# Kernel tuning notes

Measured on AMD Instinct MI355X. Metric: run time of the kernel, lower is better.

Reference implementation:

```python
import jax, jax.numpy as jnp
import numpy as np

N_NODES = 100000
N_EDGES = 400000
F_IN = 128
HEADS = 4
C1 = 64   # conv1 out per head
C2 = 128  # conv2 out per head
G = 2048  # num graphs
FP = 2048
HID = 64
NEG_SLOPE = 0.2


def _gat_conv(x, edge_index, W, a_src, a_dst, b, heads, ch):
    """PyG-style GATConv with self-loops, concat=True."""
    n = x.shape[0]
    loops = jnp.arange(n, dtype=edge_index.dtype)
    src = jnp.concatenate([edge_index[0], loops])
    dst = jnp.concatenate([edge_index[1], loops])
    h = (x @ W).reshape(n, heads, ch)                      # [N,H,C]
    e_src = jnp.sum(h * a_src, axis=-1)                    # [N,H]
    e_dst = jnp.sum(h * a_dst, axis=-1)                    # [N,H]
    logits = jax.nn.leaky_relu(e_src[src] + e_dst[dst], NEG_SLOPE)  # [E,H]
    m = jax.ops.segment_max(logits, dst, num_segments=n)   # per-dst max
    p = jnp.exp(logits - m[dst])
    denom = jax.ops.segment_sum(p, dst, num_segments=n)
    alpha = p / denom[dst]                                 # [E,H]
    out = jax.ops.segment_sum(h[src] * alpha[:, :, None], dst, num_segments=n)
    return out.reshape(n, heads * ch) + b


def setup_inputs() -> dict:
    key = jax.random.key(0)
    ks = jax.random.split(key, 16)
    s = 0.05
    inp = {
        "x": jax.random.normal(ks[0], (N_NODES, F_IN), jnp.float32),
        "edge_index": jax.random.randint(ks[1], (2, N_EDGES), 0, N_NODES, jnp.int32),
        "batch": jnp.sort(jax.random.randint(ks[2], (N_NODES,), 0, G, jnp.int32)),
        "fp": jax.random.normal(ks[3], (G, FP), jnp.float32),
        "W1": jax.random.normal(ks[4], (F_IN, HEADS * C1), jnp.float32) * s,
        "a_src1": jax.random.normal(ks[5], (HEADS, C1), jnp.float32) * s,
        "a_dst1": jax.random.normal(ks[6], (HEADS, C1), jnp.float32) * s,
        "b1": jnp.zeros((HEADS * C1,), jnp.float32),
        "W2": jax.random.normal(ks[7], (HEADS * C1, HEADS * C2), jnp.float32) * s,
        "a_src2": jax.random.normal(ks[8], (HEADS, C2), jnp.float32) * s,
        "a_dst2": jax.random.normal(ks[9], (HEADS, C2), jnp.float32) * s,
        "b2": jnp.zeros((HEADS * C2,), jnp.float32),
        "Wfp": jax.random.normal(ks[10], (FP, HID), jnp.float32) * s,
        "bfp": jnp.zeros((HID,), jnp.float32),
        "Wfc1": jax.random.normal(ks[11], (HEADS * C2 + HID, HID), jnp.float32) * s,
        "bfc1": jnp.zeros((HID,), jnp.float32),
        "Wfc2": jax.random.normal(ks[12], (HID, 1), jnp.float32) * s,
        "bfc2": jnp.zeros((1,), jnp.float32),
    }
    return inp


def reference(x, edge_index, batch, fp, W1, a_src1, a_dst1, b1, W2, a_src2, a_dst2, b2,
              Wfp, bfp, Wfc1, bfc1, Wfc2, bfc2):
    h = _gat_conv(x, edge_index, W1, a_src1, a_dst1, b1, HEADS, C1)
    h = jax.nn.elu(h)
    h = _gat_conv(h, edge_index, W2, a_src2, a_dst2, b2, HEADS, C2)
    h = jax.nn.elu(h)
    # global mean pool over graphs
    sums = jax.ops.segment_sum(h, batch, num_segments=G)
    counts = jax.ops.segment_sum(jnp.ones((h.shape[0], 1), h.dtype), batch, num_segments=G)
    pooled = sums / jnp.maximum(counts, 1.0)               # [G, 512]
    fph = fp @ Wfp + bfp                                   # [G, 64]
    z = jnp.concatenate([pooled, fph], axis=1)             # [G, 576]
    z = jax.nn.relu(z @ Wfc1 + bfc1)
    # dropout is identity in eval mode
    return z @ Wfc2 + bfc2                                 # [G, 1]
```

## Files before the change

### kernel.cpp

```cpp
#include <hip/hip_runtime.h>
#include <math.h>

#define NEG_SLOPE 0.2f

typedef __attribute__((ext_vector_type(8))) short bf16x8;
typedef __attribute__((ext_vector_type(4))) float f32x4;
typedef __attribute__((ext_vector_type(2))) float f32x2;

__device__ __forceinline__ float b2f(short s) {
  return __uint_as_float(((unsigned int)(unsigned short)s) << 16);
}
__device__ __forceinline__ unsigned short f2b_rne(float f) {
  unsigned int u = __float_as_uint(f);
  u = (u + 0x7FFF + ((u >> 16) & 1)) >> 16;
  return (unsigned short)u;
}

__device__ __forceinline__ void fp8x8_to_f32(uint2 raw, float* f) {
  f32x2 a = __builtin_amdgcn_cvt_pk_f32_fp8((int)raw.x, false);
  f32x2 b = __builtin_amdgcn_cvt_pk_f32_fp8((int)raw.x, true);
  f32x2 c = __builtin_amdgcn_cvt_pk_f32_fp8((int)raw.y, false);
  f32x2 d = __builtin_amdgcn_cvt_pk_f32_fp8((int)raw.y, true);
  f[0] = a[0]; f[1] = a[1]; f[2] = b[0]; f[3] = b[1];
  f[4] = c[0]; f[5] = c[1]; f[6] = d[0]; f[7] = d[1];
}

__device__ __forceinline__ void acc8_fp8(uint2 raw, float a, f32x2* acc2) {
  f32x2 w2; w2[0] = a; w2[1] = a;
  acc2[0] = __builtin_elementwise_fma(w2, __builtin_amdgcn_cvt_pk_f32_fp8((int)raw.x, false), acc2[0]);
  acc2[1] = __builtin_elementwise_fma(w2, __builtin_amdgcn_cvt_pk_f32_fp8((int)raw.x, true),  acc2[1]);
  acc2[2] = __builtin_elementwise_fma(w2, __builtin_amdgcn_cvt_pk_f32_fp8((int)raw.y, false), acc2[2]);
  acc2[3] = __builtin_elementwise_fma(w2, __builtin_amdgcn_cvt_pk_f32_fp8((int)raw.y, true),  acc2[3]);
}

__device__ __forceinline__ void gload16(const unsigned short* g, unsigned short* l) {
  __builtin_amdgcn_global_load_lds(
      (const __attribute__((address_space(1))) unsigned int*)g,
      (__attribute__((address_space(3))) unsigned int*)l, 16, 0, 0);
}

template<int N> __device__ __forceinline__ void vmwait() {
  asm volatile("s_waitcnt vmcnt(%0)" :: "n"(N) : "memory");
}

__device__ __forceinline__ unsigned int bsel(uint4 d, int s) {
  return ((d.x >> (8 * s)) & 0xffu) | (((d.y >> (8 * s)) & 0xffu) << 8)
       | (((d.z >> (8 * s)) & 0xffu) << 16) | (((d.w >> (8 * s)) & 0xffu) << 24);
}

__device__ __forceinline__ void tr_one(const float* __restrict__ W,
                                       unsigned short* __restrict__ WT,
                                       int K, int N, int idx)
{
  if (idx < K * N) {
    int k = idx / N, n = idx - k * N;
    WT[(size_t)n * K + k] = f2b_rne(W[idx]);
  }
}

__global__ __launch_bounds__(256) void prep_all(
    const float* __restrict__ x, unsigned short* __restrict__ xb, size_t nx, int B0,
    const float* __restrict__ fp, unsigned short* __restrict__ fpb, size_t nf, int B1,
    const float* __restrict__ W1, unsigned short* __restrict__ W1T,
    const float* __restrict__ W2, unsigned short* __restrict__ W2T,
    const float* __restrict__ Wfp, unsigned short* __restrict__ WfpT,
    const float* __restrict__ Wfc1, unsigned short* __restrict__ Wfc1T)
{
  int b = blockIdx.x;
  const int t = threadIdx.x;
  if (b < B0) {
    size_t i = (size_t)b * 256 + t;
    if (i < nx) xb[i] = f2b_rne(x[i]);
    return;
  }
  b -= B0;
  if (b < B1) {
    size_t i = (size_t)b * 256 + t;
    if (i < nf) fpb[i] = f2b_rne(fp[i]);
    return;
  }
  b -= B1;
  if (b < 128) { tr_one(W1, W1T, 128, 256, b * 256 + t); return; }
  b -= 128;
  if (b < 512) { tr_one(W2, W2T, 256, 512, b * 256 + t); return; }
  b -= 512;
  if (b < 512) { tr_one(Wfp, WfpT, 2048, 64, b * 256 + t); return; }
  b -= 512;
  tr_one(Wfc1, Wfc1T, 576, 64, b * 256 + t);
}

__global__ __launch_bounds__(256) void prep_e(
    const float* __restrict__ W1, const float* __restrict__ as1, const float* __restrict__ ad1,
    const float* __restrict__ W2, const float* __restrict__ as2, const float* __restrict__ ad2,
    unsigned short* __restrict__ BeT1, unsigned short* __restrict__ BeT2)
{
  const int b = blockIdx.x;
  const int k = threadIdx.x;
  if (b < 4) {
    if (k < 128) {
      float ss = 0.f, sd = 0.f;
      for (int c = 0; c < 64; ++c) {
        float w = W1[k * 256 + b * 64 + c];
        ss += w * as1[b * 64 + c];
        sd += w * ad1[b * 64 + c];
      }
      BeT1[b * 128 + k] = f2b_rne(ss);
      BeT1[(4 + b) * 128 + k] = f2b_rne(sd);
    }
  } else {
    const int h = b - 4;
    float ss = 0.f, sd = 0.f;
    for (int c = 0; c < 128; ++c) {
      float w = W2[k * 512 + h * 128 + c];
      ss += w * as2[h * 128 + c];
      sd += w * ad2[h * 128 + c];
    }
    BeT2[h * 256 + k] = f2b_rne(ss);
    BeT2[(4 + h) * 256 + k] = f2b_rne(sd);
  }
}

template<int KK>
__global__ __launch_bounds__(256) void gemm_mfma(
    const unsigned short* __restrict__ A, const unsigned short* __restrict__ BT,
    unsigned char* __restrict__ Cout, int M, int N,
    const unsigned short* __restrict__ BeT,
    float* __restrict__ es, float* __restrict__ ed, int nh)
{
  constexpr int NT = KK / 32;
  constexpr int LDE = KK + 8;
  __shared__ unsigned short As[4][128 * 32];
  __shared__ unsigned short Bs[4][128 * 32];
  __shared__ unsigned short Be[16 * LDE];
  const int tid  = threadIdx.x;
  const int wave = tid >> 6;
  const int lane = tid & 63;
  const int ln   = lane & 15;
  const int quad = lane >> 4;
  const int wr0  = (wave >> 1) * 64;
  const int wc0  = (wave & 1) * 64;

  const int nwg = gridDim.x;
  const int ncol = N >> 7;
  const int bid = blockIdx.x;
  const int qq = nwg >> 3, rr = nwg & 7;
  const int xc = bid & 7, io = bid >> 3;
  const int swz = (xc < rr ? xc * (qq + 1) : rr * (qq + 1) + (xc - rr) * qq) + io;
  const int bn = (swz % ncol) * 128;
  const int bm = (swz / ncol) * 128;
  const bool do_e = (bn == 0) && (wc0 == 0);

  if (bn == 0 && tid < KK) {
    const int rrw = tid / (KK / 8);
    const int ccl = (tid % (KK / 8)) * 8;
    bf16x8 v = *(const bf16x8*)(BeT + rrw * KK + ccl);
    *(bf16x8*)(&Be[rrw * LDE + ccl]) = v;
  }
  __syncthreads();

  const int srow = lane >> 2;
  const int cch  = lane & 3;
  const int rt0  = wave * 32 + srow;
  const int ksw  = ((cch ^ (srow & 3)) << 3);
  int ar0 = bm + rt0;      if (ar0 >= M) ar0 = M - 1;
  int ar1 = bm + rt0 + 16; if (ar1 >= M) ar1 = M - 1;
  const unsigned short* gA0 = A + (size_t)ar0 * KK + ksw;
  const unsigned short* gA1 = A + (size_t)ar1 * KK + ksw;
  const unsigned short* gB0 = BT + (size_t)(bn + rt0) * KK + ksw;
  const unsigned short* gB1 = BT + (size_t)(bn + rt0 + 16) * KK + ksw;

  auto stage = [&](int T) {
    const int b = T & 3;
    const int kk = T * 32;
    gload16(gA0 + kk, &As[b][(wave * 32) * 32]);
    gload16(gA1 + kk, &As[b][(wave * 32 + 16) * 32]);
    gload16(gB0 + kk, &Bs[b][(wave * 32) * 32]);
    gload16(gB1 + kk, &Bs[b][(wave * 32 + 16) * 32]);
  };

  f32x4 acc[4][4];
  f32x4 acc_e[4];
  const f32x4 z4 = {0.f, 0.f, 0.f, 0.f};
#pragma unroll
  for (int i = 0; i < 4; ++i) {
    acc_e[i] = z4;
#pragma unroll
    for (int j = 0; j < 4; ++j) acc[i][j] = z4;
  }

  stage(0); stage(1); stage(2);

#pragma unroll
  for (int t = 0; t < NT; ++t) {
    if (t + 3 < NT) stage(t + 3);
    if      (t < NT - 3) vmwait<12>();
    else if (t == NT - 3) vmwait<8>();
    else if (t == NT - 2) vmwait<4>();
    else                  vmwait<0>();
    __builtin_amdgcn_s_barrier();
    __builtin_amdgcn_sched_barrier(0);
    const int b = t & 3;
    bf16x8 af[4], bfv[4];
#pragma unroll
    for (int i = 0; i < 4; ++i) {
      const int row = wr0 + i * 16 + ln;
      af[i] = *(const bf16x8*)(&As[b][row * 32 + ((quad ^ (ln & 3)) << 3)]);
    }
#pragma unroll
    for (int j = 0; j < 4; ++j) {
      const int row = wc0 + j * 16 + ln;
      bfv[j] = *(const bf16x8*)(&Bs[b][row * 32 + ((quad ^ (ln & 3)) << 3)]);
    }
#pragma unroll
    for (int i = 0; i < 4; ++i)
#pragma unroll
      for (int j = 0; j < 4; ++j)
        acc[i][j] = __builtin_amdgcn_mfma_f32_16x16x32_bf16(af[i], bfv[j], acc[i][j], 0, 0, 0);
    if (do_e) {
      bf16x8 bfe = *(const bf16x8*)(&Be[ln * LDE + t * 32 + quad * 8]);
#pragma unroll
      for (int i = 0; i < 4; ++i)
        acc_e[i] = __builtin_amdgcn_mfma_f32_16x16x32_bf16(af[i], bfe, acc_e[i], 0, 0, 0);
    }
    __builtin_amdgcn_sched_barrier(0);
    __builtin_amdgcn_s_barrier();
  }
  __syncthreads();

  unsigned int* Cb = (unsigned int*)As;
  const int cbase = (wc0 >> 2) + ln;
#pragma unroll
  for (int i = 0; i < 4; ++i) {
#pragma unroll
    for (int r = 0; r < 4; ++r) {
      int rowl = wr0 + i * 16 + quad * 4 + r;
      int p = __builtin_amdgcn_cvt_pk_fp8_f32(acc[i][0][r], acc[i][1][r], 0, false);
      p     = __builtin_amdgcn_cvt_pk_fp8_f32(acc[i][2][r], acc[i][3][r], p, true);
      Cb[rowl * 36 + cbase] = (unsigned int)p;
    }
  }
  if (do_e) {
#pragma unroll
    for (int i = 0; i < 4; ++i) {
#pragma unroll
      for (int r = 0; r < 4; ++r) {
        int row = bm + wr0 + i * 16 + quad * 4 + r;
        if (row < M && ln < 8) {
          float* dst = (ln < 4) ? es : ed;
          dst[(size_t)row * nh + (ln & 3)] = acc_e[i][r];
        }
      }
    }
  }
  __syncthreads();

  {
    const int rT = tid >> 1;
    const int hT = tid & 1;
    const unsigned int* cp = &Cb[rT * 36 + 16 * hT];
    uint4 d0 = *(const uint4*)(cp + 0);
    uint4 d1 = *(const uint4*)(cp + 4);
    uint4 d2 = *(const uint4*)(cp + 8);
    uint4 d3 = *(const uint4*)(cp + 12);
    int grow = bm + rT;
    if (grow < M) {
      unsigned char* gp = Cout + (size_t)grow * N + bn + 64 * hT;
      uint4 o;
      o.x = bsel(d0, 0); o.y = bsel(d1, 0); o.z = bsel(d2, 0); o.w = bsel(d3, 0);
      *(uint4*)(gp + 0) = o;
      o.x = bsel(d0, 1); o.y = bsel(d1, 1); o.z = bsel(d2, 1); o.w = bsel(d3, 1);
      *(uint4*)(gp + 16) = o;
      o.x = bsel(d0, 2); o.y = bsel(d1, 2); o.z = bsel(d2, 2); o.w = bsel(d3, 2);
      *(uint4*)(gp + 32) = o;
      o.x = bsel(d0, 3); o.y = bsel(d1, 3); o.z = bsel(d2, 3); o.w = bsel(d3, 3);
      *(uint4*)(gp + 48) = o;
    }
  }
}

__global__ __launch_bounds__(256) void gemm_mfma_n64(
    const unsigned short* __restrict__ A, int lda,
    const unsigned short* __restrict__ BT, int ldb,
    float* __restrict__ Cp, int M, int kchunk)
{
  const int LDT = 72;
  __shared__ unsigned short As[128 * 72];
  __shared__ unsigned short Bs[64 * 72];
  const int tid  = threadIdx.x;
  const int wave = tid >> 6;
  const int lane = tid & 63;
  const int ln   = lane & 15;
  const int quad = lane >> 4;
  const int ks   = blockIdx.x;
  const int bm   = blockIdx.y * 128;
  const int k_beg = ks * kchunk;
  const int k_end = k_beg + kchunk;
  const int arow = tid >> 1;
  const int akb  = (tid & 1) * 32;
  const int brow = tid >> 2;
  const int bkb  = (tid & 3) * 16;

  f32x4 acc[2][4];
  const f32x4 z4 = {0.f, 0.f, 0.f, 0.f};
#pragma unroll
  for (int i = 0; i < 2; ++i)
#pragma unroll
    for (int j = 0; j < 4; ++j) acc[i][j] = z4;

  for (int k0 = k_beg; k0 < k_end; k0 += 64) {
    const unsigned short* ap = A + (size_t)(bm + arow) * lda + k0 + akb;
#pragma unroll
    for (int q = 0; q < 4; ++q)
      *(bf16x8*)(&As[arow * LDT + akb + q * 8]) = *(const bf16x8*)(ap + q * 8);
    const unsigned short* bp = BT + (size_t)brow * ldb + k0 + bkb;
#pragma unroll
    for (int q = 0; q < 2; ++q)
      *(bf16x8*)(&Bs[brow * LDT + bkb + q * 8]) = *(const bf16x8*)(bp + q * 8);
    __syncthreads();
#pragma unroll
    for (int kk = 0; kk < 2; ++kk) {
      bf16x8 af[2], bfv[4];
#pragma unroll
      for (int i = 0; i < 2; ++i)
        af[i] = *(const bf16x8*)(&As[(wave * 32 + i * 16 + ln) * LDT + kk * 32 + quad * 8]);
#pragma unroll
      for (int j = 0; j < 4; ++j)
        bfv[j] = *(const bf16x8*)(&Bs[(j * 16 + ln) * LDT + kk * 32 + quad * 8]);
#pragma unroll
      for (int i = 0; i < 2; ++i)
#pragma unroll
        for (int j = 0; j < 4; ++j)
          acc[i][j] = __builtin_amdgcn_mfma_f32_16x16x32_bf16(af[i], bfv[j], acc[i][j], 0, 0, 0);
    }
    __syncthreads();
  }
#pragma unroll
  for (int i = 0; i < 2; ++i)
#pragma unroll
    for (int r = 0; r < 4; ++r) {
      int row = bm + wave * 32 + i * 16 + quad * 4 + r;
#pragma unroll
      for (int j = 0; j < 4; ++j)
        Cp[((size_t)ks * M + row) * 64 + j * 16 + ln] = acc[i][j][r];
    }
}

__global__ void fp_finish(const float* __restrict__ Cp, int ksplit, int M,
                          const float* __restrict__ bfp,
                          unsigned short* __restrict__ zb)
{
  const int g = blockIdx.x;
  const int j = threadIdx.x;
  float s = bfp[j];
  for (int ks = 0; ks < ksplit; ++ks) s += Cp[((size_t)ks * M + g) * 64 + j];
  zb[(size_t)g * 576 + 512 + j] = f2b_rne(s);
}

__global__ void mlp_finish(const float* __restrict__ Cp, int ksplit, int M,
                           const float* __restrict__ bfc1,
                           const float* __restrict__ Wfc2, const float* __restrict__ bfc2,
                           float* __restrict__ out)
{
  const int g = blockIdx.x;
  const int j = threadIdx.x;
  float s = bfc1[j];
  for (int ks = 0; ks < ksplit; ++ks) s += Cp[((size_t)ks * M + g) * 64 + j];
  s = s > 0.f ? s : 0.f;
  float term = s * Wfc2[j];
  for (int off = 32; off; off >>= 1) term += __shfl_down(term, off, 64);
  if (j == 0) out[g] = term + bfc2[0];
}

__global__ void count_all(const int* __restrict__ ei, int E, int* __restrict__ deg,
                          const int* __restrict__ batch, int NN, int* __restrict__ gcnt,
                          int BE)
{
  int b = blockIdx.x;
  int t = threadIdx.x;
  if (b < BE) {
    int e = b * 256 + t;
    if (e < E) atomicAdd(&deg[ei[E + e]], 1);
  } else {
    int i = (b - BE) * 256 + t;
    if (i < NN) atomicAdd(&gcnt[batch[i]], 1);
  }
}

__global__ void fill_csr(const int* __restrict__ ei, int E, int* __restrict__ cursor,
                         const int* __restrict__ rowptr, int* __restrict__ csr_src)
{
  int e = blockIdx.x * 256 + threadIdx.x;
  if (e < E) {
    int d = ei[E + e];
    int pos = atomicAdd(&cursor[d], 1);
    csr_src[rowptr[d] + pos] = ei[e];
  }
}

__device__ void scan_p1_body(const int* __restrict__ vals, int n, int* __restrict__ bsum,
                             int bb)
{
  __shared__ int red[256];
  int base = bb * 1024;
  int t = threadIdx.x;
  int s = 0;
#pragma unroll
  for (int i = 0; i < 4; ++i) {
    int idx = base + i * 256 + t;
    if (idx < n) s += vals[idx];
  }
  red[t] = s;
  __syncthreads();
  for (int off = 128; off; off >>= 1) {
    if (t < off) red[t] += red[t + off];
    __syncthreads();
  }
  if (t == 0) bsum[bb] = red[0];
}

__global__ void scan2_p1(const int* __restrict__ vA, int nA, int* __restrict__ bsA, int nbA,
                         const int* __restrict__ vB, int nB, int* __restrict__ bsB)
{
  int b = blockIdx.x;
  if (b < nbA) scan_p1_body(vA, nA, bsA, b);
  else         scan_p1_body(vB, nB, bsB, b - nbA);
}

__device__ void scan_p2_body(const int* __restrict__ bsum, int* __restrict__ bpre,
                             int nb, int* __restrict__ rowptr, int n)
{
  __shared__ int tmp[128];
  int t = threadIdx.x;
  int v = (t < nb) ? bsum[t] : 0;
  tmp[t] = v;
  __syncthreads();
  for (int off = 1; off < 128; off <<= 1) {
    int add = (t >= off) ? tmp[t - off] : 0;
    __syncthreads();
    tmp[t] += add;
    __syncthreads();
  }
  if (t < nb) bpre[t] = tmp[t] - v;
  if (t == 127) rowptr[n] = tmp[127];
}

__global__ void scan2_p2(const int* __restrict__ bsA, int* __restrict__ bpA, int nbA,
                         int* __restrict__ rpA, int nA,
                         const int* __restrict__ bsB, int* __restrict__ bpB, int nbB,
                         int* __restrict__ rpB, int nB)
{
  if (blockIdx.x == 0) scan_p2_body(bsA, bpA, nbA, rpA, nA);
  else                 scan_p2_body(bsB, bpB, nbB, rpB, nB);
}

__device__ void scan_p3_body(const int* __restrict__ vals, const int* __restrict__ bpre,
                             int n, int* __restrict__ rowptr, int bb)
{
  __shared__ int tmp[256];
  int t = threadIdx.x;
  int base = bb * 1024 + t * 4;
  int v[4]; int s = 0;
#pragma unroll
  for (int i = 0; i < 4; ++i) {
    int idx = base + i;
    v[i] = (idx < n) ? vals[idx] : 0;
    s += v[i];
  }
  tmp[t] = s;
  __syncthreads();
  for (int off = 1; off < 256; off <<= 1) {
    int add = (t >= off) ? tmp[t - off] : 0;
    __syncthreads();
    tmp[t] += add;
    __syncthreads();
  }
  int run = bpre[bb] + tmp[t] - s;
#pragma unroll
  for (int i = 0; i < 4; ++i) {
    int idx = base + i;
    if (idx < n) rowptr[idx] = run;
    run += v[i];
  }
}

__global__ void scan2_p3(const int* __restrict__ vA, const int* __restrict__ bpA, int nA,
                         int* __restrict__ rpA, int nbA,
                         const int* __restrict__ vB, const int* __restrict__ bpB, int nB,
                         int* __restrict__ rpB)
{
  int b = blockIdx.x;
  if (b < nbA) scan_p3_body(vA, bpA, nA, rpA, b);
  else         scan_p3_body(vB, bpB, nB, rpB, b - nbA);
}

__global__ void alpha_kernel(const float* __restrict__ es, const float* __restrict__ ed,
                             const int* __restrict__ rowptr, const int* __restrict__ csr_src,
                             float* __restrict__ w_csr, float* __restrict__ wself,
                             float* __restrict__ dinv, int N, int nh)
{
  int idx = blockIdx.x * 256 + threadIdx.x;
  if (idx >= N * nh) return;
  const int dst = idx / nh;
  const int h = idx - dst * nh;
  const float edh = ed[(size_t)dst * nh + h];
  const int beg = rowptr[dst], end = rowptr[dst + 1];
  float sum = 0.f;
  for (int e = beg; e < end; ++e) {
    int s = csr_src[e];
    float l = es[(size_t)s * nh + h] + edh;
    l = l >= 0.f ? l : NEG_SLOPE * l;
    float w = expf(l);
    w_csr[(size_t)e * nh + h] = w;
    sum += w;
  }
  float ls = es[(size_t)dst * nh + h] + edh;
  ls = ls >= 0.f ? ls : NEG_SLOPE * ls;
  float wsl = expf(ls);
  sum += wsl;
  wself[(size_t)dst * nh + h] = wsl;
  dinv[(size_t)dst * nh + h] = 1.0f / sum;
}

__global__ __launch_bounds__(256) void aggregate_b(
    const unsigned char* __restrict__ h,
    const float* __restrict__ w_csr, const float* __restrict__ wself,
    const float* __restrict__ dinv,
    const int* __restrict__ rowptr, const int* __restrict__ csr_src,
    const float* __restrict__ bias, unsigned short* __restrict__ out,
    int N, int nh, int C)
{
  const int HC = nh * C;
  const int CH8 = HC >> 3;
  const int dpb = 256 / CH8;
  const int grp = threadIdx.x / CH8;
  const int lane = threadIdx.x - grp * CH8;
  const int dst = blockIdx.x * dpb + grp;
  if (dst >= N) return;
  const int ch = lane << 3;
  const int head = ch / C;
  const int beg = rowptr[dst], end = rowptr[dst + 1];
  f32x2 acc2[4];
#pragma unroll
  for (int q = 0; q < 4; ++q) { acc2[q][0] = 0.f; acc2[q][1] = 0.f; }
  int e = beg;
  for (; e + 3 < end; e += 4) {
    int s0 = csr_src[e], s1 = csr_src[e + 1], s2 = csr_src[e + 2], s3 = csr_src[e + 3];
    float a0 = w_csr[(size_t)e * nh + head];
    float a1 = w_csr[(size_t)(e + 1) * nh + head];
    float a2 = w_csr[(size_t)(e + 2) * nh + head];
    float a3 = w_csr[(size_t)(e + 3) * nh + head];
    uint2 r0 = *(const uint2*)(h + (size_t)s0 * HC + ch);
    uint2 r1 = *(const uint2*)(h + (size_t)s1 * HC + ch);
    uint2 r2 = *(const uint2*)(h + (size_t)s2 * HC + ch);
    uint2 r3 = *(const uint2*)(h + (size_t)s3 * HC + ch);
    acc8_fp8(r0, a0, acc2); acc8_fp8(r1, a1, acc2);
    acc8_fp8(r2, a2, acc2); acc8_fp8(r3, a3, acc2);
  }
  for (; e < end; ++e) {
    int s0 = csr_src[e];
    float a0 = w_csr[(size_t)e * nh + head];
    uint2 r0 = *(const uint2*)(h + (size_t)s0 * HC + ch);
    acc8_fp8(r0, a0, acc2);
  }
  {
    float a = wself[(size_t)dst * nh + head];
    uint2 r0 = *(const uint2*)(h + (size_t)dst * HC + ch);
    acc8_fp8(r0, a, acc2);
  }
  const float di = dinv[(size_t)dst * nh + head];
  bf16x8 o;
#pragma unroll
  for (int q = 0; q < 4; ++q) {
#pragma unroll
    for (int u = 0; u < 2; ++u) {
      float v = acc2[q][u] * di + bias[ch + q * 2 + u];
      v = v > 0.f ? v : (expf(v) - 1.0f);
      o[q * 2 + u] = (short)f2b_rne(v);
    }
  }
  *(bf16x8*)(out + (size_t)dst * HC + ch) = o;
}

__global__ __launch_bounds__(512) void agg_pool(
    const unsigned char* __restrict__ h,
    const float* __restrict__ w_csr, const float* __restrict__ wself,
    const float* __restrict__ dinv,
    const int* __restrict__ rowptr, const int* __restrict__ csr_src,
    const float* __restrict__ bias, const int* __restrict__ grp,
    unsigned short* __restrict__ zb)
{
  const int g = blockIdx.x;
  const int wave = threadIdx.x >> 6;
  const int lane = threadIdx.x & 63;
  const int ch = lane << 3;
  const int head = lane >> 4;
  const int gbeg = grp[g], gend = grp[g + 1];
  float bch[8];
#pragma unroll
  for (int r = 0; r < 8; ++r) bch[r] = bias[ch + r];
  f32x2 pool2[4];
#pragma unroll
  for (int q = 0; q < 4; ++q) { pool2[q][0] = 0.f; pool2[q][1] = 0.f; }

  for (int node = gbeg + wave; node < gend; node += 8) {
    const int beg = rowptr[node], end = rowptr[node + 1];
    f32x2 acc2[4];
#pragma unroll
    for (int q = 0; q < 4; ++q) { acc2[q][0] = 0.f; acc2[q][1] = 0.f; }
    int e = beg;
    for (; e + 3 < end; e += 4) {
      int s0 = csr_src[e], s1 = csr_src[e + 1], s2 = csr_src[e + 2], s3 = csr_src[e + 3];
      float a0 = w_csr[(size_t)e * 4 + head];
      float a1 = w_csr[(size_t)(e + 1) * 4 + head];
      float a2 = w_csr[(size_t)(e + 2) * 4 + head];
      float a3 = w_csr[(size_t)(e + 3) * 4 + head];
      uint2 r0 = *(const uint2*)(h + (size_t)s0 * 512 + ch);
      uint2 r1 = *(const uint2*)(h + (size_t)s1 * 512 + ch);
      uint2 r2 = *(const uint2*)(h + (size_t)s2 * 512 + ch);
      uint2 r3 = *(const uint2*)(h + (size_t)s3 * 512 + ch);
      acc8_fp8(r0, a0, acc2); acc8_fp8(r1, a1, acc2);
      acc8_fp8(r2, a2, acc2); acc8_fp8(r3, a3, acc2);
    }
    for (; e < end; ++e) {
      int s0 = csr_src[e];
      float a0 = w_csr[(size_t)e * 4 + head];
      uint2 r0 = *(const uint2*)(h + (size_t)s0 * 512 + ch);
      acc8_fp8(r0, a0, acc2);
    }
    {
      float a = wself[(size_t)node * 4 + head];
      uint2 r0 = *(const uint2*)(h + (size_t)node * 512 + ch);
      acc8_fp8(r0, a, acc2);
    }
    const float di = dinv[(size_t)node * 4 + head];
#pragma unroll
    for (int q = 0; q < 4; ++q) {
#pragma unroll
      for (int u = 0; u < 2; ++u) {
        float v = acc2[q][u] * di + bch[q * 2 + u];
        v = v > 0.f ? v : (expf(v) - 1.0f);
        pool2[q][u] += v;
      }
    }
  }

  __shared__ float red[8][512];
#pragma unroll
  for (int q = 0; q < 4; ++q) {
    red[wave][ch + 2 * q]     = pool2[q][0];
    red[wave][ch + 2 * q + 1] = pool2[q][1];
  }
  __syncthreads();
  const float inv = 1.0f / (float)max(gend - gbeg, 1);
  {
    const int c = threadIdx.x;
    float s = 0.f;
#pragma unroll
    for (int w = 0; w < 8; ++w) s += red[w][c];
    zb[(size_t)g * 576 + c] = f2b_rne(s * inv);
  }
}

extern "C" void kernel_launch(void* const* d_in, const int* in_sizes, int n_in,
                              void* d_out, int out_size, void* d_ws, size_t ws_size,
                              hipStream_t stream)
{
  const float* x      = (const float*)d_in[0];
  const int*   ei     = (const int*)d_in[1];
  const int*   batch  = (const int*)d_in[2];
  const float* fp     = (const float*)d_in[3];
  const float* W1     = (const float*)d_in[4];
  const float* a_src1 = (const float*)d_in[5];
  const float* a_dst1 = (const float*)d_in[6];
  const float* b1     = (const float*)d_in[7];
  const float* W2     = (const float*)d_in[8];
  const float* a_src2 = (const float*)d_in[9];
  const float* a_dst2 = (const float*)d_in[10];
  const float* b2     = (const float*)d_in[11];
  const float* Wfp    = (const float*)d_in[12];
  const float* bfp    = (const float*)d_in[13];
  const float* Wfc1   = (const float*)d_in[14];
  const float* bfc1   = (const float*)d_in[15];
  const float* Wfc2   = (const float*)d_in[16];
  const float* bfc2   = (const float*)d_in[17];
  float* out = (float*)d_out;

  const int NN = in_sizes[0] / 128;
  const int E  = in_sizes[1] / 2;
  const int G  = in_sizes[3] / 2048;
  const int FIN = 128, H = 4, C1 = 64, C2 = 128;
  const int HC1 = H * C1;
  const int HC2 = H * C2;
  const int KFP = in_sizes[3] / G;
  const int KZ  = HC2 + 64;
  const int KS_FP = 16;
  const int KS_Z  = 9;

  char* base = (char*)d_ws;
  size_t off = 0;
  auto alloc = [&](size_t bytes) {
    char* p = base + off; off += (bytes + 255) & ~(size_t)255; return p;
  };
  size_t xb_sz  = ((size_t)NN * FIN * 2 + 255) & ~(size_t)255;
  size_t h1b_sz = (size_t)NN * HC1;
  size_t h2b_sz = (size_t)NN * HC2;
  size_t rA = xb_sz + h1b_sz; if (h2b_sz > rA) rA = h2b_sz;
  char* RA = alloc(rA);
  unsigned short* xb  = (unsigned short*)RA;
  unsigned char*  h1b = (unsigned char*)(RA + xb_sz);
  unsigned char*  h2b = (unsigned char*)RA;
  size_t fpb_sz  = ((size_t)G * KFP * 2 + 255) & ~(size_t)255;
  size_t cpfp_sz = (size_t)KS_FP * G * 64 * 4;
  size_t agg1_sz = (size_t)NN * HC1 * 2;
  size_t rB = fpb_sz + cpfp_sz; if (agg1_sz > rB) rB = agg1_sz;
  char* RB = alloc(rB);
  unsigned short* fpb   = (unsigned short*)RB;
  float*          Cp_fp = (float*)(RB + fpb_sz);
  unsigned short* agg1b = (unsigned short*)RB;
  float* w1     = (float*)alloc((size_t)E * H * 4);
  float* wself1 = (float*)alloc((size_t)NN * H * 4);
  float* es1    = (float*)alloc((size_t)NN * H * 4);
  float* ed1    = (float*)alloc((size_t)NN * H * 4);
  float* dinv1  = (float*)alloc((size_t)NN * H * 4);
  float* w2 = w1, *wself2 = wself1, *es2 = es1, *ed2 = ed1, *dinv2 = dinv1;
  unsigned short* zb    = (unsigned short*)alloc((size_t)G * KZ * 2);
  float*          Cp_z  = (float*)alloc((size_t)KS_Z * G * 64 * 4);
  unsigned short* W1T   = (unsigned short*)alloc((size_t)HC1 * FIN * 2);
  unsigned short* W2T   = (unsigned short*)alloc((size_t)HC2 * HC1 * 2);
  unsigned short* WfpT  = (unsigned short*)alloc((size_t)64 * KFP * 2);
  unsigned short* Wfc1T = (unsigned short*)alloc((size_t)64 * KZ * 2);
  unsigned short* BeT1  = (unsigned short*)alloc((size_t)8 * 128 * 2);
  unsigned short* BeT2  = (unsigned short*)alloc((size_t)8 * 256 * 2);
  int* iarena   = (int*)alloc(((size_t)2 * NN + G) * 4);
  int* deg      = iarena;
  int* cursor   = iarena + NN;
  int* gcnt     = iarena + 2 * NN;
  int* rowptr_n = (int*)alloc(((size_t)NN + 1) * 4);
  int* rowptr_g = (int*)alloc(((size_t)G + 1) * 4);
  int* csr_src  = (int*)alloc((size_t)E * 4);
  int* bsumA    = (int*)alloc(128 * 4);
  int* bpreA    = (int*)alloc(128 * 4);
  int* bsumB    = (int*)alloc(128 * 4);
  int* bpreB    = (int*)alloc(128 * 4);

  const size_t nx = (size_t)NN * FIN;
  const size_t nf = (size_t)G * KFP;
  const int B0 = (int)((nx + 255) / 256);
  const int B1 = (int)((nf + 255) / 256);
  {
    int nb = B0 + B1 + 128 + 512 + 512 + 144;
    prep_all<<<nb, 256, 0, stream>>>(x, xb, nx, B0, fp, fpb, nf, B1,
                                     W1, W1T, W2, W2T, Wfp, WfpT, Wfc1, Wfc1T);
  }
  prep_e<<<8, 256, 0, stream>>>(W1, a_src1, a_dst1, W2, a_src2, a_dst2, BeT1, BeT2);

  {
    dim3 gg(KS_FP, G / 128);
    gemm_mfma_n64<<<gg, 256, 0, stream>>>(fpb, KFP, WfpT, KFP, Cp_fp, G, KFP / KS_FP);
    fp_finish<<<G, 64, 0, stream>>>(Cp_fp, KS_FP, G, bfp, zb);
  }

  hipMemsetAsync(iarena, 0, sizeof(int) * ((size_t)2 * NN + G), stream);
  {
    int BE = (E + 255) / 256;
    int BN = (NN + 255) / 256;
    count_all<<<BE + BN, 256, 0, stream>>>(ei, E, deg, batch, NN, gcnt, BE);
  }
  {
    int nbA = (NN + 1023) / 1024;
    int nbB = (G + 1023) / 1024;
    scan2_p1<<<nbA + nbB, 256, 0, stream>>>(deg, NN, bsumA, nbA, gcnt, G, bsumB);
    scan2_p2<<<2, 128, 0, stream>>>(bsumA, bpreA, nbA, rowptr_n, NN,
                                    bsumB, bpreB, nbB, rowptr_g, G);
    scan2_p3<<<nbA + nbB, 256, 0, stream>>>(deg, bpreA, NN, rowptr_n, nbA,
                                            gcnt, bpreB, G, rowptr_g);
  }
  fill_csr<<<(E + 255) / 256, 256, 0, stream>>>(ei, E, cursor, rowptr_n, csr_src);

  {
    const int nrow = (NN + 127) / 128;
    gemm_mfma<128><<<nrow * (HC1 / 128), 256, 0, stream>>>(
        xb, W1T, h1b, NN, HC1, BeT1, es1, ed1, H);
  }
  alpha_kernel<<<(NN * H + 255) / 256, 256, 0, stream>>>(es1, ed1, rowptr_n, csr_src,
                                                         w1, wself1, dinv1, NN, H);
  aggregate_b<<<(NN + 7) / 8, 256, 0, stream>>>(h1b, w1, wself1, dinv1, rowptr_n, csr_src,
                                                b1, agg1b, NN, H, C1);

  {
    const int nrow = (NN + 127) / 128;
    gemm_mfma<256><<<nrow * (HC2 / 128), 256, 0, stream>>>(
        agg1b, W2T, h2b, NN, HC2, BeT2, es2, ed2, H);
  }
  alpha_kernel<<<(NN * H + 255) / 256, 256, 0, stream>>>(es2, ed2, rowptr_n, csr_src,
                                                         w2, wself2, dinv2, NN, H);
  agg_pool<<<G, 512, 0, stream>>>(h2b, w2, wself2, dinv2, rowptr_n, csr_src,
                                  b2, rowptr_g, zb);

  {
    dim3 gg(KS_Z, G / 128);
    gemm_mfma_n64<<<gg, 256, 0, stream>>>(zb, KZ, Wfc1T, KZ, Cp_z, G, KZ / KS_Z);
    mlp_finish<<<G, 64, 0, stream>>>(Cp_z, KS_Z, G, bfc1, Wfc2, bfc2, out);
  }
}
```

Measured before the change: 474.9 us.

## Split pooled aggregation into fixed node chunks with atomic per-graph accumulation

Replaces the one-block-per-graph aggregate+pool kernel with blocks over fixed 32-node chunks, where each wave accumulates ELU outputs and flushes them to a float pool buffer with atomicAdd whenever the graph id changes. A separate finish kernel divides by node counts and writes bf16 into the MLP input. This targets load imbalance from variable graph sizes (about 49 nodes per graph, 8 waves per block) and gives a more uniform grid. In exchange it adds float atomics, a memset, an extra launch, and sums in an order that is not deterministic.

```diff
diff --git a/kernel.cpp b/kernel.cpp
--- a/kernel.cpp
+++ b/kernel.cpp
@@ -14,15 +14,6 @@
   unsigned int u = __float_as_uint(f);
   u = (u + 0x7FFF + ((u >> 16) & 1)) >> 16;
   return (unsigned short)u;
-}
-
-__device__ __forceinline__ void fp8x8_to_f32(uint2 raw, float* f) {
-  f32x2 a = __builtin_amdgcn_cvt_pk_f32_fp8((int)raw.x, false);
-  f32x2 b = __builtin_amdgcn_cvt_pk_f32_fp8((int)raw.x, true);
-  f32x2 c = __builtin_amdgcn_cvt_pk_f32_fp8((int)raw.y, false);
-  f32x2 d = __builtin_amdgcn_cvt_pk_f32_fp8((int)raw.y, true);
-  f[0] = a[0]; f[1] = a[1]; f[2] = b[0]; f[3] = b[1];
-  f[4] = c[0]; f[5] = c[1]; f[6] = d[0]; f[7] = d[1];
 }
 
 __device__ __forceinline__ void acc8_fp8(uint2 raw, float a, f32x2* acc2) {
@@ -581,28 +572,44 @@
   *(bf16x8*)(out + (size_t)dst * HC + ch) = o;
 }
 
-__global__ __launch_bounds__(512) void agg_pool(
+#define NPB 32
+__global__ __launch_bounds__(256) void agg_pool_atomic(
     const unsigned char* __restrict__ h,
     const float* __restrict__ w_csr, const float* __restrict__ wself,
     const float* __restrict__ dinv,
     const int* __restrict__ rowptr, const int* __restrict__ csr_src,
-    const float* __restrict__ bias, const int* __restrict__ grp,
-    unsigned short* __restrict__ zb)
-{
-  const int g = blockIdx.x;
+    const float* __restrict__ bias, const int* __restrict__ batch,
+    float* __restrict__ pool, int NN)
+{
   const int wave = threadIdx.x >> 6;
   const int lane = threadIdx.x & 63;
   const int ch = lane << 3;
   const int head = lane >> 4;
-  const int gbeg = grp[g], gend = grp[g + 1];
+  const int base = blockIdx.x * NPB;
   float bch[8];
 #pragma unroll
   for (int r = 0; r < 8; ++r) bch[r] = bias[ch + r];
   f32x2 pool2[4];
 #pragma unroll
   for (int q = 0; q < 4; ++q) { pool2[q][0] = 0.f; pool2[q][1] = 0.f; }
-
-  for (int node = gbeg + wave; node < gend; node += 8) {
+  int cur_g = -1;
+
+  const int lim = (base + NPB < NN) ? base + NPB : NN;
+  for (int node = base + wave; node < lim; node += 4) {
+    const int g = batch[node];
+    if (g != cur_g) {
+      if (cur_g >= 0) {
+        float* pg = pool + (size_t)cur_g * 512 + ch;
+#pragma unroll
+        for (int q = 0; q < 4; ++q) {
+          atomicAdd(pg + 2 * q,     pool2[q][0]);
+          atomicAdd(pg + 2 * q + 1, pool2[q][1]);
+        }
+#pragma unroll
+        for (int q = 0; q < 4; ++q) { pool2[q][0] = 0.f; pool2[q][1] = 0.f; }
+      }
+      cur_g = g;
+    }
     const int beg = rowptr[node], end = rowptr[node + 1];
     f32x2 acc2[4];
 #pragma unroll
@@ -643,22 +650,24 @@
       }
     }
   }
-
-  __shared__ float red[8][512];
-#pragma unroll
-  for (int q = 0; q < 4; ++q) {
-    red[wave][ch + 2 * q]     = pool2[q][0];
-    red[wave][ch + 2 * q + 1] = pool2[q][1];
-  }
-  __syncthreads();
-  const float inv = 1.0f / (float)max(gend - gbeg, 1);
-  {
-    const int c = threadIdx.x;
-    float s = 0.f;
-#pragma unroll
-    for (int w = 0; w < 8; ++w) s += red[w][c];
-    zb[(size_t)g * 576 + c] = f2b_rne(s * inv);
-  }
+  if (cur_g >= 0) {
+    float* pg = pool + (size_t)cur_g * 512 + ch;
+#pragma unroll
+    for (int q = 0; q < 4; ++q) {
+      atomicAdd(pg + 2 * q,     pool2[q][0]);
+      atomicAdd(pg + 2 * q + 1, pool2[q][1]);
+    }
+  }
+}
+
+__global__ void pool_finish(const float* __restrict__ pool, const int* __restrict__ rpg,
+                            unsigned short* __restrict__ zb)
+{
+  const int g = blockIdx.x;
+  const int c = threadIdx.x;
+  const int cnt = rpg[g + 1] - rpg[g];
+  const float inv = 1.0f / (float)(cnt > 1 ? cnt : 1);
+  zb[(size_t)g * 576 + c] = f2b_rne(pool[(size_t)g * 512 + c] * inv);
 }
 
 extern "C" void kernel_launch(void* const* d_in, const int* in_sizes, int n_in,
@@ -725,6 +734,7 @@
   float* w2 = w1, *wself2 = wself1, *es2 = es1, *ed2 = ed1, *dinv2 = dinv1;
   unsigned short* zb    = (unsigned short*)alloc((size_t)G * KZ * 2);
   float*          Cp_z  = (float*)alloc((size_t)KS_Z * G * 64 * 4);
+  float*          pool  = (float*)alloc((size_t)G * HC2 * 4);
   unsigned short* W1T   = (unsigned short*)alloc((size_t)HC1 * FIN * 2);
   unsigned short* W2T   = (unsigned short*)alloc((size_t)HC2 * HC1 * 2);
   unsigned short* WfpT  = (unsigned short*)alloc((size_t)64 * KFP * 2);
@@ -743,6 +753,8 @@
   int* bsumB    = (int*)alloc(128 * 4);
   int* bpreB    = (int*)alloc(128 * 4);
 
+  hipMemsetAsync(pool, 0, (size_t)G * HC2 * 4, stream);
+
   const size_t nx = (size_t)NN * FIN;
   const size_t nf = (size_t)G * KFP;
   const int B0 = (int)((nx + 255) / 256);
@@ -794,8 +806,9 @@
   }
   alpha_kernel<<<(NN * H + 255) / 256, 256, 0, stream>>>(es2, ed2, rowptr_n, csr_src,
                                                          w2, wself2, dinv2, NN, H);
-  agg_pool<<<G, 512, 0, stream>>>(h2b, w2, wself2, dinv2, rowptr_n, csr_src,
-                                  b2, rowptr_g, zb);
+  agg_pool_atomic<<<(NN + NPB - 1) / NPB, 256, 0, stream>>>(
+      h2b, w2, wself2, dinv2, rowptr_n, csr_src, b2, batch, pool, NN);
+  pool_finish<<<G, 512, 0, stream>>>(pool, rowptr_g, zb);
 
   {
     dim3 gg(KS_Z, G / 128);
```

Measured after the change: 693.0 us. +45.9%, slower.
